# Performance work log

Hardware: AMD Instinct MI355X
Metric: run time of the kernel (lower is better)

## Reference

```python
import jax, jax.numpy as jnp
import numpy as np

N_HEAD = 16
D_HEAD = 64
D_MODEL = 1024
D_INNER = 4096
QLEN = 1024
MLEN = 1024
BSZ = 2
LN_EPS = 1e-5


def _layer_norm(x, g, b, eps=LN_EPS):
    mu = jnp.mean(x, axis=-1, keepdims=True)
    var = jnp.var(x, axis=-1, keepdims=True)
    return (x - mu) * jax.lax.rsqrt(var + eps) * g + b


def _rel_shift(x):
    # x: [qlen, rlen, bsz, n_head]
    q, r, b, n = x.shape
    zp = jnp.zeros((q, 1, b, n), x.dtype)
    xp = jnp.concatenate([zp, x], axis=1).reshape(r + 1, q, b, n)
    return xp[1:].reshape(q, r, b, n)


def setup_inputs() -> dict:
    key = jax.random.key(0)
    ks = jax.random.split(key, 12)
    klen = MLEN + QLEN
    w = jax.random.normal(ks[0], (QLEN, BSZ, D_MODEL), jnp.float32)
    r = jax.random.normal(ks[1], (klen, D_MODEL), jnp.float32)
    mems = jax.random.normal(ks[2], (MLEN, BSZ, D_MODEL), jnp.float32)
    # causal mask: query i attends keys j <= i + mlen
    i = jnp.arange(QLEN)[:, None]
    j = jnp.arange(klen)[None, :]
    attn_mask = (j > i + MLEN)[:, :, None]  # [qlen, klen, 1] bool
    s = 0.02
    params = dict(
        qkv_w=jax.random.normal(ks[3], (3 * N_HEAD * D_HEAD, D_MODEL), jnp.float32) * s,
        r_net_w=jax.random.normal(ks[4], (N_HEAD * D_HEAD, D_MODEL), jnp.float32) * s,
        o_w=jax.random.normal(ks[5], (D_MODEL, N_HEAD * D_HEAD), jnp.float32) * s,
        r_r_bias=jax.random.normal(ks[6], (N_HEAD, D_HEAD), jnp.float32) * s,
        r_w_bias=jax.random.normal(ks[7], (N_HEAD, D_HEAD), jnp.float32) * s,
        ln1_g=jnp.ones((D_MODEL,), jnp.float32),
        ln1_b=jnp.zeros((D_MODEL,), jnp.float32),
        ff_w1=jax.random.normal(ks[8], (D_INNER, D_MODEL), jnp.float32) * s,
        ff_b1=jnp.zeros((D_INNER,), jnp.float32),
        ff_w2=jax.random.normal(ks[9], (D_MODEL, D_INNER), jnp.float32) * s,
        ff_b2=jnp.zeros((D_MODEL,), jnp.float32),
        ln2_g=jnp.ones((D_MODEL,), jnp.float32),
        ln2_b=jnp.zeros((D_MODEL,), jnp.float32),
    )
    return dict(w=w, r=r, mems=mems, attn_mask=attn_mask, **params)


def reference(w, r, mems, attn_mask, qkv_w, r_net_w, o_w, r_r_bias, r_w_bias,
              ln1_g, ln1_b, ff_w1, ff_b1, ff_w2, ff_b2, ln2_g, ln2_b):
    qlen, bsz = w.shape[0], w.shape[1]
    scale = 1.0 / (D_HEAD ** 0.5)
    cat = jnp.concatenate([mems, w], axis=0)              # [klen, b, d_model]
    klen = cat.shape[0]
    w_heads = cat @ qkv_w.T                                # [klen, b, 3*n*d]
    wq, wk, wv = jnp.split(w_heads, 3, axis=-1)
    wq = wq[-qlen:]
    r_head_k = (r @ r_net_w.T).reshape(-1, N_HEAD, D_HEAD)  # [rlen, n, d]
    wq = wq.reshape(qlen, bsz, N_HEAD, D_HEAD)
    wk = wk.reshape(klen, bsz, N_HEAD, D_HEAD)
    wv = wv.reshape(klen, bsz, N_HEAD, D_HEAD)
    AC = jnp.einsum('ibnd,jbnd->ijbn', wq + r_w_bias, wk)   # content term
    BD = jnp.einsum('ibnd,jnd->ijbn', wq + r_r_bias, r_head_k)
    BD = _rel_shift(BD)                                     # position term
    attn_score = (AC + BD) * scale
    mask_value = jnp.finfo(attn_score.dtype).min
    attn_score = jnp.where(attn_mask[:, :, :, None], mask_value, attn_score)
    attn_prob = jax.nn.softmax(attn_score, axis=1)
    attn_vec = jnp.einsum('ijbn,jbnd->ibnd', attn_prob, wv)
    attn_vec = attn_vec.reshape(qlen, bsz, N_HEAD * D_HEAD)
    attn_out = attn_vec @ o_w.T
    h = _layer_norm(w + attn_out, ln1_g, ln1_b)             # post-lnorm
    core = jax.nn.relu(h @ ff_w1.T + ff_b1) @ ff_w2.T + ff_b2
    out = _layer_norm(h + core, ln2_g, ln2_b)
    return out
```

## Files before the change

kernel.cpp:

```cpp
#include <hip/hip_runtime.h>
#include <math.h>

#define QLEN 1024
#define MLEN 1024
#define KLEN 2048
#define BSZc 2
#define NH 16
#define DH 64
#define DM 1024
#define DI 4096

typedef unsigned short ushort_t;
typedef __attribute__((ext_vector_type(8))) short short8;
typedef __attribute__((ext_vector_type(4))) float f32x4;

__device__ __forceinline__ ushort_t f2bf(float x) {
    unsigned int u = __float_as_uint(x);
    unsigned int r = (u + 0x7FFFu + ((u >> 16) & 1u)) >> 16;
    return (ushort_t)r;
}

__device__ __forceinline__ void gload_lds16(const ushort_t* g, ushort_t* l) {
    __builtin_amdgcn_global_load_lds(
        (const __attribute__((address_space(1))) unsigned int*)g,
        (__attribute__((address_space(3))) unsigned int*)l,
        16, 0, 0);
}

__device__ __forceinline__ void cast8(const float* s, ushort_t* d, int g) {
    const float4 a = *(const float4*)(s + g * 8);
    const float4 b = *(const float4*)(s + g * 8 + 4);
    short8 o;
    o[0] = (short)f2bf(a.x); o[1] = (short)f2bf(a.y);
    o[2] = (short)f2bf(a.z); o[3] = (short)f2bf(a.w);
    o[4] = (short)f2bf(b.x); o[5] = (short)f2bf(b.y);
    o[6] = (short)f2bf(b.z); o[7] = (short)f2bf(b.w);
    *(short8*)(d + g * 8) = o;
}

__global__ __launch_bounds__(256)
void cast_phase1(const float* __restrict__ qkv_w, const float* __restrict__ rnet_w,
                 const float* __restrict__ mems, const float* __restrict__ w,
                 const float* __restrict__ r,
                 ushort_t* __restrict__ W1, ushort_t* __restrict__ W2,
                 ushort_t* __restrict__ Acat, ushort_t* __restrict__ Rsrc)
{
    int g = blockIdx.x * 256 + threadIdx.x;
    if (g < 393216)            { cast8(qkv_w,  W1,              g); }
    else if (g < 524288)       { cast8(rnet_w, W2,              g - 393216); }
    else if (g < 786432)       { cast8(mems,   Acat,            g - 524288); }
    else if (g < 1048576)      { cast8(w,      Acat + 2097152,  g - 786432); }
    else if (g < 1310720)      { cast8(r,      Rsrc,            g - 1048576); }
}

__global__ __launch_bounds__(256)
void cast_phase2(const float* __restrict__ o_w, const float* __restrict__ ffw1,
                 const float* __restrict__ ffw2,
                 ushort_t* __restrict__ W3, ushort_t* __restrict__ W4,
                 ushort_t* __restrict__ W5)
{
    int g = blockIdx.x * 256 + threadIdx.x;
    if (g < 131072)            { cast8(o_w,  W3, g); }
    else if (g < 655360)       { cast8(ffw1, W4, g - 131072); }
    else if (g < 1179648)      { cast8(ffw2, W5, g - 655360); }
}

template<int EMODE, int ACT, int BN, int SPLIT>
__global__ __launch_bounds__(256)
void gemm_mfma(const ushort_t* __restrict__ A, const ushort_t* __restrict__ B,
               const float* __restrict__ bias,
               void* __restrict__ O0v, void* __restrict__ O1v,
               int M, int N, int Ks, int lda, int ldb)
{
    constexpr int JT = BN / 32;
    __shared__ ushort_t At0[128 * 32];
    __shared__ ushort_t At1[128 * 32];
    __shared__ ushort_t Bt0[BN * 32];
    __shared__ ushort_t Bt1[BN * 32];

    const int tid  = threadIdx.x;
    const int lane = tid & 63;
    const int w    = tid >> 6;
    const int lr   = lane & 15;
    const int quad = lane >> 4;
    const int m0   = blockIdx.x * 128;
    const int n0   = blockIdx.y * BN;
    const int z    = (SPLIT > 1) ? (int)blockIdx.z : 0;
    const int kbase = z * Ks;
    const int wm0  = (w >> 1) * 64;
    const int wn0  = (w & 1) * (BN / 2);

    f32x4 acc[4][JT];
#pragma unroll
    for (int it = 0; it < 4; ++it)
#pragma unroll
        for (int jt = 0; jt < JT; ++jt) acc[it][jt] = (f32x4){0.f, 0.f, 0.f, 0.f};

    const int srow = lane >> 2;
    const int scol = (lane & 3) << 3;
    const ushort_t* Ag = A + (size_t)(m0 + w * 32 + srow) * lda + kbase + scol;
    ushort_t* a00 = At0 + (w * 32) * 32;
    ushort_t* a01 = At0 + (w * 32 + 16) * 32;
    ushort_t* a10 = At1 + (w * 32) * 32;
    ushort_t* a11 = At1 + (w * 32 + 16) * 32;
    const ushort_t* Bg;
    ushort_t *b00, *b01 = nullptr, *b10, *b11 = nullptr;
    if (BN == 128) {
        Bg  = B + (size_t)(n0 + w * 32 + srow) * ldb + kbase + scol;
        b00 = Bt0 + (w * 32) * 32;
        b01 = Bt0 + (w * 32 + 16) * 32;
        b10 = Bt1 + (w * 32) * 32;
        b11 = Bt1 + (w * 32 + 16) * 32;
    } else {
        Bg  = B + (size_t)(n0 + w * 16 + srow) * ldb + kbase + scol;
        b00 = Bt0 + (w * 16) * 32;
        b10 = Bt1 + (w * 16) * 32;
    }

    const ushort_t* Ato0 = At0 + (wm0 + lr) * 32 + quad * 8;
    const ushort_t* Ato1 = At1 + (wm0 + lr) * 32 + quad * 8;
    const ushort_t* Bto0 = Bt0 + (wn0 + lr) * 32 + quad * 8;
    const ushort_t* Bto1 = Bt1 + (wn0 + lr) * 32 + quad * 8;

    for (int k0 = 0; k0 < Ks; k0 += 64) {
        __syncthreads();
        gload_lds16(Ag + k0, a00);
        gload_lds16(Ag + (size_t)16 * lda + k0, a01);
        gload_lds16(Ag + k0 + 32, a10);
        gload_lds16(Ag + (size_t)16 * lda + k0 + 32, a11);
        if (BN == 128) {
            gload_lds16(Bg + k0, b00);
            gload_lds16(Bg + (size_t)16 * ldb + k0, b01);
            gload_lds16(Bg + k0 + 32, b10);
            gload_lds16(Bg + (size_t)16 * ldb + k0 + 32, b11);
        } else {
            gload_lds16(Bg + k0, b00);
            gload_lds16(Bg + k0 + 32, b10);
        }
        __syncthreads();

        short8 af[4], bf[JT];
#pragma unroll
        for (int it = 0; it < 4; ++it)
            af[it] = *(const short8*)(Ato0 + it * 16 * 32);
#pragma unroll
        for (int jt = 0; jt < JT; ++jt)
            bf[jt] = *(const short8*)(Bto0 + jt * 16 * 32);
#pragma unroll
        for (int it = 0; it < 4; ++it)
#pragma unroll
            for (int jt = 0; jt < JT; ++jt)
                acc[it][jt] = __builtin_amdgcn_mfma_f32_16x16x32_bf16(
                    af[it], bf[jt], acc[it][jt], 0, 0, 0);
#pragma unroll
        for (int it = 0; it < 4; ++it)
            af[it] = *(const short8*)(Ato1 + it * 16 * 32);
#pragma unroll
        for (int jt = 0; jt < JT; ++jt)
            bf[jt] = *(const short8*)(Bto1 + jt * 16 * 32);
#pragma unroll
        for (int it = 0; it < 4; ++it)
#pragma unroll
            for (int jt = 0; jt < JT; ++jt)
                acc[it][jt] = __builtin_amdgcn_mfma_f32_16x16x32_bf16(
                    af[it], bf[jt], acc[it][jt], 0, 0, 0);
    }

#pragma unroll
    for (int it = 0; it < 4; ++it)
#pragma unroll
        for (int jt = 0; jt < JT; ++jt)
#pragma unroll
            for (int rg = 0; rg < 4; ++rg) {
                const int m = m0 + wm0 + it * 16 + quad * 4 + rg;
                const int n = n0 + wn0 + jt * 16 + lr;
                float v = acc[it][jt][rg];
                if (EMODE == 0) {
                    float* dst = (float*)(z ? O1v : O0v);
                    if (bias && z == 0) v += bias[n];
                    dst[(size_t)m * N + n] = v;
                } else {
                    v += bias[n];
                    if (ACT == 1) v = fmaxf(v, 0.f);
                    ((ushort_t*)O0v)[(size_t)m * N + n] = f2bf(v);
                }
            }
}

__global__ __launch_bounds__(256)
void gemm_qkvr(const ushort_t* __restrict__ Acat, const ushort_t* __restrict__ W1,
               const ushort_t* __restrict__ Rsrc, const ushort_t* __restrict__ W2,
               ushort_t* __restrict__ Qac, ushort_t* __restrict__ Qbd,
               ushort_t* __restrict__ Kbf, ushort_t* __restrict__ Vtb,
               ushort_t* __restrict__ Rh,
               const float* __restrict__ rwb, const float* __restrict__ rrb)
{
    __shared__ ushort_t At0[128 * 32];
    __shared__ ushort_t At1[128 * 32];
    __shared__ ushort_t Bt0[128 * 32];
    __shared__ ushort_t Bt1[128 * 32];

    const int bid  = blockIdx.x;
    const bool isr = bid >= 768;
    const ushort_t* A; const ushort_t* B; int m0, n0;
    if (!isr) { A = Acat; B = W1; m0 = (bid & 31) * 128; n0 = (bid >> 5) * 128; }
    else { int t = bid - 768; A = Rsrc; B = W2; m0 = (t & 15) * 128; n0 = (t >> 4) * 128; }
    const int K = 1024;

    const int tid  = threadIdx.x;
    const int lane = tid & 63;
    const int w    = tid >> 6;
    const int lr   = lane & 15;
    const int quad = lane >> 4;
    const int wm0  = (w >> 1) * 64;
    const int wn0  = (w & 1) * 64;

    f32x4 acc[4][4];
#pragma unroll
    for (int it = 0; it < 4; ++it)
#pragma unroll
        for (int jt = 0; jt < 4; ++jt) acc[it][jt] = (f32x4){0.f, 0.f, 0.f, 0.f};

    const int srow = lane >> 2;
    const int scol = (lane & 3) << 3;
    const ushort_t* Ag = A + (size_t)(m0 + w * 32 + srow) * K + scol;
    const ushort_t* Bg = B + (size_t)(n0 + w * 32 + srow) * K + scol;
    ushort_t* a00 = At0 + (w * 32) * 32;
    ushort_t* a01 = At0 + (w * 32 + 16) * 32;
    ushort_t* a10 = At1 + (w * 32) * 32;
    ushort_t* a11 = At1 + (w * 32 + 16) * 32;
    ushort_t* b00 = Bt0 + (w * 32) * 32;
    ushort_t* b01 = Bt0 + (w * 32 + 16) * 32;
    ushort_t* b10 = Bt1 + (w * 32) * 32;
    ushort_t* b11 = Bt1 + (w * 32 + 16) * 32;

    const ushort_t* Ato0 = At0 + (wm0 + lr) * 32 + quad * 8;
    const ushort_t* Ato1 = At1 + (wm0 + lr) * 32 + quad * 8;
    const ushort_t* Bto0 = Bt0 + (wn0 + lr) * 32 + quad * 8;
    const ushort_t* Bto1 = Bt1 + (wn0 + lr) * 32 + quad * 8;

    for (int k0 = 0; k0 < K; k0 += 64) {
        __syncthreads();
        gload_lds16(Ag + k0, a00);
        gload_lds16(Ag + (size_t)16 * K + k0, a01);
        gload_lds16(Ag + k0 + 32, a10);
        gload_lds16(Ag + (size_t)16 * K + k0 + 32, a11);
        gload_lds16(Bg + k0, b00);
        gload_lds16(Bg + (size_t)16 * K + k0, b01);
        gload_lds16(Bg + k0 + 32, b10);
        gload_lds16(Bg + (size_t)16 * K + k0 + 32, b11);
        __syncthreads();

        short8 af[4], bf[4];
#pragma unroll
        for (int it = 0; it < 4; ++it)
            af[it] = *(const short8*)(Ato0 + it * 16 * 32);
#pragma unroll
        for (int jt = 0; jt < 4; ++jt)
            bf[jt] = *(const short8*)(Bto0 + jt * 16 * 32);
#pragma unroll
        for (int it = 0; it < 4; ++it)
#pragma unroll
            for (int jt = 0; jt < 4; ++jt)
                acc[it][jt] = __builtin_amdgcn_mfma_f32_16x16x32_bf16(
                    af[it], bf[jt], acc[it][jt], 0, 0, 0);
#pragma unroll
        for (int it = 0; it < 4; ++it)
            af[it] = *(const short8*)(Ato1 + it * 16 * 32);
#pragma unroll
        for (int jt = 0; jt < 4; ++jt)
            bf[jt] = *(const short8*)(Bto1 + jt * 16 * 32);
#pragma unroll
        for (int it = 0; it < 4; ++it)
#pragma unroll
            for (int jt = 0; jt < 4; ++jt)
                acc[it][jt] = __builtin_amdgcn_mfma_f32_16x16x32_bf16(
                    af[it], bf[jt], acc[it][jt], 0, 0, 0);
    }

#pragma unroll
    for (int it = 0; it < 4; ++it)
#pragma unroll
        for (int jt = 0; jt < 4; ++jt)
#pragma unroll
            for (int rg = 0; rg < 4; ++rg) {
                const int m = m0 + wm0 + it * 16 + quad * 4 + rg;
                const int n = n0 + wn0 + jt * 16 + lr;
                const float v = acc[it][jt][rg];
                if (!isr) {
                    const int j = m >> 1, b = m & 1;
                    const int part = n >> 10, hh = (n >> 6) & 15, d = n & 63;
                    if (part == 0) {
                        if (j >= MLEN) {
                            const int qi = j - MLEN;
                            const size_t qidx = (((size_t)(b * NH + hh)) * QLEN + qi) * DH + d;
                            Qac[qidx] = f2bf(v + rwb[hh * DH + d]);
                            Qbd[qidx] = f2bf(v + rrb[hh * DH + d]);
                        }
                    } else if (part == 1) {
                        Kbf[(((size_t)(b * NH + hh)) * KLEN + j) * DH + d] = f2bf(v);
                    } else {
                        Vtb[(((size_t)(b * NH + hh)) * DH + d) * KLEN + j] = f2bf(v);
                    }
                } else {
                    const int hh = n >> 6, d = n & 63;
                    Rh[(((size_t)hh) * KLEN + m) * DH + d] = f2bf(v);
                }
            }
}

__global__ __launch_bounds__(256, 3)
void attn_mfma(const ushort_t* __restrict__ Qac, const ushort_t* __restrict__ Qbd,
               const ushort_t* __restrict__ Kb, const ushort_t* __restrict__ Vt,
               const ushort_t* __restrict__ Rb,
               float* __restrict__ OpA, float* __restrict__ OpB,
               float* __restrict__ Mp, float* __restrict__ Lp)
{
    __shared__ __align__(16) ushort_t Kt[64 * 64];
    __shared__ __align__(16) ushort_t Rt[128 * 64];
    __shared__ __align__(16) float    Bw[4][16][84];

    const int tid  = threadIdx.x;
    const int lane = tid & 63;
    const int w    = tid >> 6;
    const int lr   = lane & 15;
    const int quad = lane >> 4;
    const int d    = blockIdx.x;
    const int L    = (d & 7) * 224 + (d >> 3);
    const int bh   = L / 56;
    const int r    = L % 56;
    int qt, z;
    if (r < 32) { qt = 15 - (r >> 2); z = r & 3; }
    else        { int r2 = r - 32; int q3 = r2 / 3; qt = 7 - q3; z = r2 - q3 * 3; }
    const int i0   = qt << 6;
    const int h    = bh & 15;
    const int b    = bh >> 4;

    short8 qaf[2], qbf[2];
    {
        const size_t rowoff = ((size_t)bh * QLEN + i0 + w * 16 + lr) * DH;
#pragma unroll
        for (int kt = 0; kt < 2; ++kt) {
            qaf[kt] = *(const short8*)(Qac + rowoff + kt * 32 + quad * 8);
            qbf[kt] = *(const short8*)(Qbd + rowoff + kt * 32 + quad * 8);
        }
    }

    f32x4 O[4];
#pragma unroll
    for (int nt = 0; nt < 4; ++nt) O[nt] = (f32x4){0.f, 0.f, 0.f, 0.f};
    float m_run = -3.4e38f, l_run = 0.f;

    const int nc   = qt + 17;
    const int c_lo = z * 8;
    const int c_hi = (c_lo + 8 < nc) ? (c_lo + 8) : nc;
    const int stw  = 3 - w;
    const float SC = 0.125f * 1.44269504f;
    const ushort_t* Kh  = Kb + (size_t)bh * KLEN * DH;
    const ushort_t* Vh  = Vt + (size_t)bh * DH * KLEN;
    const ushort_t* Rhp = Rb + (size_t)h * KLEN * DH;

    const int lrow = lane >> 3;
    const int lsg  = lane & 7;
    const int sgo  = (lsg ^ lrow) << 3;
    const int xq   = lr & 7;
    const int fo0  = ((quad ^ xq)) << 3;
    const int fo1  = (((4 | quad) ^ xq)) << 3;

    {
        const int j0 = c_lo << 6;
        const int wb = 960 - i0 + j0;
#pragma unroll
        for (int t = 0; t < 2; ++t) {
            const int rb  = t * 32 + w * 8;
            gload_lds16(Kh + (size_t)(j0 + rb + lrow) * DH + sgo,
                        Kt + rb * 64);
        }
#pragma unroll
        for (int t = 0; t < 4; ++t) {
            const int gb = wb + t * 32 + w * 8;
            const int g  = gb + lrow;
            const int gc = g > (KLEN - 1) ? (KLEN - 1) : g;
            gload_lds16(Rhp + (size_t)gc * DH + sgo,
                        Rt + (gb & 127) * 64);
        }
    }

    for (int c = c_lo; c < c_hi; ++c) {
        const int j0 = c << 6;
        const int wb = 960 - i0 + j0;

        __syncthreads();

        short8 vpf[2][4];
#pragma unroll
        for (int kt = 0; kt < 2; ++kt)
#pragma unroll
            for (int nt = 0; nt < 4; ++nt)
                vpf[kt][nt] = *(const short8*)(
                    Vh + (size_t)(nt * 16 + lr) * KLEN + j0 + kt * 32 + quad * 8);

#pragma unroll
        for (int ctl = 0; ctl < 5; ++ctl) {
            const int wr = (stw + ctl) * 16 + lr;
            const int ring = (wb + wr) & 127;
            f32x4 zz = (f32x4){0.f, 0.f, 0.f, 0.f};
            short8 r0 = *(const short8*)&Rt[ring * 64 + fo0];
            zz = __builtin_amdgcn_mfma_f32_16x16x32_bf16(qbf[0], r0, zz, 0, 0, 0);
            short8 r1 = *(const short8*)&Rt[ring * 64 + fo1];
            zz = __builtin_amdgcn_mfma_f32_16x16x32_bf16(qbf[1], r1, zz, 0, 0, 0);
#pragma unroll
            for (int rg = 0; rg < 4; ++rg)
                Bw[w][quad * 4 + rg][ctl * 16 + lr] = zz[rg];
        }
#pragma unroll
        for (int ct = 0; ct < 4; ++ct) {
            f32x4 zz = (f32x4){0.f, 0.f, 0.f, 0.f};
            short8 k0f = *(const short8*)&Kt[(ct * 16 + lr) * 64 + fo0];
            zz = __builtin_amdgcn_mfma_f32_16x16x32_bf16(qaf[0], k0f, zz, 0, 0, 0);
            short8 k1f = *(const short8*)&Kt[(ct * 16 + lr) * 64 + fo1];
            zz = __builtin_amdgcn_mfma_f32_16x16x32_bf16(qaf[1], k1f, zz, 0, 0, 0);
#pragma unroll
            for (int rg = 0; rg < 4; ++rg) {
                const int rrow = quad * 4 + rg;
                Bw[w][rrow][ct * 16 + lr + 15 - rrow] += zz[rg];
            }
        }

        const int lim = i0 + w * 16 + lr + 1024 - j0;
        float pv[16];
        float mx = -3.4e38f;
#pragma unroll
        for (int kt = 0; kt < 2; ++kt)
#pragma unroll
            for (int t = 0; t < 8; ++t) {
                const int jj = kt * 32 + quad * 8 + t;
                float sv = Bw[w][lr][jj + 15 - lr] * SC;
                sv = (jj > lim) ? -3.4e38f : sv;
                pv[kt * 8 + t] = sv;
                mx = fmaxf(mx, sv);
            }
        mx = fmaxf(mx, __shfl_xor(mx, 16, 64));
        mx = fmaxf(mx, __shfl_xor(mx, 32, 64));
        const float m_new = fmaxf(m_run, mx);
        float ps = 0.f;
        short8 pf[2];
#pragma unroll
        for (int kt = 0; kt < 2; ++kt)
#pragma unroll
            for (int t = 0; t < 8; ++t) {
                const float e = exp2f(pv[kt * 8 + t] - m_new);
                ps += e;
                pf[kt][t] = (short)f2bf(e);
            }
        ps += __shfl_xor(ps, 16, 64);
        ps += __shfl_xor(ps, 32, 64);
        const float alpha = exp2f(m_run - m_new);
        m_run = m_new;
        l_run = l_run * alpha + ps;

        __syncthreads();

        if (c + 1 < c_hi) {
            const int j1 = j0 + 64;
#pragma unroll
            for (int t = 0; t < 2; ++t) {
                const int rb = t * 32 + w * 8;
                gload_lds16(Kh + (size_t)(j1 + rb + lrow) * DH + sgo,
                            Kt + rb * 64);
            }
#pragma unroll
            for (int t = 0; t < 2; ++t) {
                const int gb = wb + 128 + t * 32 + w * 8;
                const int g  = gb + lrow;
                const int gc = g > (KLEN - 1) ? (KLEN - 1) : g;
                gload_lds16(Rhp + (size_t)gc * DH + sgo,
                            Rt + (gb & 127) * 64);
            }
        }

        float ar[4];
#pragma unroll
        for (int rg = 0; rg < 4; ++rg)
            ar[rg] = __shfl(alpha, quad * 4 + rg, 64);
#pragma unroll
        for (int nt = 0; nt < 4; ++nt) {
            O[nt][0] *= ar[0]; O[nt][1] *= ar[1];
            O[nt][2] *= ar[2]; O[nt][3] *= ar[3];
        }
#pragma unroll
        for (int kt = 0; kt < 2; ++kt)
#pragma unroll
            for (int nt = 0; nt < 4; ++nt)
                O[nt] = __builtin_amdgcn_mfma_f32_16x16x32_bf16(pf[kt], vpf[kt][nt], O[nt], 0, 0, 0);
    }

    if (quad == 0) {
        const size_t mi = ((size_t)(z * 32 + bh)) * QLEN + i0 + w * 16 + lr;
        Mp[mi] = m_run;
        Lp[mi] = l_run;
    }
    float* Op = (z < 2) ? (OpA + (size_t)z * 2097152)
                        : (OpB + (size_t)(z - 2) * 2097152);
#pragma unroll
    for (int nt = 0; nt < 4; ++nt)
#pragma unroll
        for (int rg = 0; rg < 4; ++rg) {
            const int i = i0 + w * 16 + quad * 4 + rg;
            Op[((size_t)i * BSZc + b) * DM + h * DH + nt * 16 + lr] = O[nt][rg];
        }
}

__global__ __launch_bounds__(256)
void attn_merge(const float* __restrict__ OpA, const float* __restrict__ OpB,
                const float* __restrict__ Mp, const float* __restrict__ Lp,
                ushort_t* __restrict__ AV)
{
    const int row = blockIdx.x;
    const int tid = threadIdx.x;
    const int i = row >> 1, b = row & 1;
    const int h = tid >> 4;
    const int bh = b * NH + h;
    const size_t mi = (size_t)bh * QLEN + i;
    const bool p4 = (i >= 512);
    const float m0 = Mp[mi],                l0 = Lp[mi];
    const float m1 = Mp[32 * QLEN + mi],    l1 = Lp[32 * QLEN + mi];
    const float m2 = Mp[64 * QLEN + mi],    l2 = Lp[64 * QLEN + mi];
    float m3 = -3.4e38f, l3 = 0.f;
    if (p4) { m3 = Mp[96 * QLEN + mi]; l3 = Lp[96 * QLEN + mi]; }
    const float M = fmaxf(fmaxf(m0, m1), fmaxf(m2, m3));
    const float a0 = exp2f(m0 - M), a1 = exp2f(m1 - M);
    const float a2 = exp2f(m2 - M), a3 = exp2f(m3 - M);
    const float rl = 1.f / (l0 * a0 + l1 * a1 + l2 * a2 + l3 * a3);
    const float f0 = a0 * rl, f1 = a1 * rl, f2 = a2 * rl, f3 = a3 * rl;
    const float4 o0 = ((const float4*)(OpA + (size_t)row * DM))[tid];
    const float4 o1 = ((const float4*)(OpA + 2097152 + (size_t)row * DM))[tid];
    const float4 o2 = ((const float4*)(OpB + (size_t)row * DM))[tid];
    float4 o3 = (float4){0.f, 0.f, 0.f, 0.f};
    if (p4) o3 = ((const float4*)(OpB + 2097152 + (size_t)row * DM))[tid];
    ushort_t* p = AV + (size_t)row * DM + tid * 4;
    p[0] = f2bf(o0.x * f0 + o1.x * f1 + o2.x * f2 + o3.x * f3);
    p[1] = f2bf(o0.y * f0 + o1.y * f1 + o2.y * f2 + o3.y * f3);
    p[2] = f2bf(o0.z * f0 + o1.z * f1 + o2.z * f2 + o3.z * f3);
    p[3] = f2bf(o0.w * f0 + o1.w * f1 + o2.w * f2 + o3.w * f3);
}

__global__ __launch_bounds__(256)
void add_ln(const float* __restrict__ X, const float* __restrict__ Y0,
            const float* __restrict__ Y1,
            const float* __restrict__ gg, const float* __restrict__ bb,
            float* __restrict__ out, ushort_t* __restrict__ outb)
{
    const int row  = blockIdx.x;
    const int tid  = threadIdx.x;
    const int lane = tid & 63;
    const int w    = tid >> 6;
    __shared__ float ssum[4], ssq[4];

    const float4 xv = ((const float4*)(X + (size_t)row * DM))[tid];
    const float4 yv = ((const float4*)(Y0 + (size_t)row * DM))[tid];
    float v0 = xv.x + yv.x, v1 = xv.y + yv.y;
    float v2 = xv.z + yv.z, v3 = xv.w + yv.w;
    if (Y1) {
        const float4 zv = ((const float4*)(Y1 + (size_t)row * DM))[tid];
        v0 += zv.x; v1 += zv.y; v2 += zv.z; v3 += zv.w;
    }
    float s = v0 + v1 + v2 + v3;
    float q = v0 * v0 + v1 * v1 + v2 * v2 + v3 * v3;
#pragma unroll
    for (int off = 32; off > 0; off >>= 1) {
        s += __shfl_xor(s, off, 64);
        q += __shfl_xor(q, off, 64);
    }
    if (lane == 0) { ssum[w] = s; ssq[w] = q; }
    __syncthreads();
    s = ssum[0] + ssum[1] + ssum[2] + ssum[3];
    q = ssq[0] + ssq[1] + ssq[2] + ssq[3];
    const float mean = s * (1.f / DM);
    const float var  = q * (1.f / DM) - mean * mean;
    const float rs   = rsqrtf(var + 1e-5f);
    const float4 g4 = ((const float4*)gg)[tid];
    const float4 b4 = ((const float4*)bb)[tid];
    float4 ov;
    ov.x = (v0 - mean) * rs * g4.x + b4.x;
    ov.y = (v1 - mean) * rs * g4.y + b4.y;
    ov.z = (v2 - mean) * rs * g4.z + b4.z;
    ov.w = (v3 - mean) * rs * g4.w + b4.w;
    ((float4*)(out + (size_t)row * DM))[tid] = ov;
    if (outb) {
        ushort_t* p = outb + (size_t)row * DM + tid * 4;
        p[0] = f2bf(ov.x); p[1] = f2bf(ov.y);
        p[2] = f2bf(ov.z); p[3] = f2bf(ov.w);
    }
}

extern "C" void kernel_launch(void* const* d_in, const int* in_sizes, int n_in,
                              void* d_out, int out_size, void* d_ws, size_t ws_size,
                              hipStream_t stream)
{
    (void)in_sizes; (void)n_in; (void)out_size; (void)ws_size;
    const float* w      = (const float*)d_in[0];
    const float* r      = (const float*)d_in[1];
    const float* mems   = (const float*)d_in[2];
    const float* qkv_w  = (const float*)d_in[4];
    const float* rnet_w = (const float*)d_in[5];
    const float* o_w    = (const float*)d_in[6];
    const float* r_r_b  = (const float*)d_in[7];
    const float* r_w_b  = (const float*)d_in[8];
    const float* ln1g   = (const float*)d_in[9];
    const float* ln1b   = (const float*)d_in[10];
    const float* ffw1   = (const float*)d_in[11];
    const float* ffb1   = (const float*)d_in[12];
    const float* ffw2   = (const float*)d_in[13];
    const float* ffb2   = (const float*)d_in[14];
    const float* ln2g   = (const float*)d_in[15];
    const float* ln2b   = (const float*)d_in[16];
    float* out = (float*)d_out;

    char* wsb = (char*)d_ws;
    const size_t MB = 1024 * 1024;
    ushort_t* W1    = (ushort_t*)(wsb + 0 * MB);
    ushort_t* W2    = (ushort_t*)(wsb + 6 * MB);
    ushort_t* Acat  = (ushort_t*)(wsb + 8 * MB);
    ushort_t* Rsrc  = (ushort_t*)(wsb + 16 * MB);
    ushort_t* Qac   = (ushort_t*)(wsb + 20 * MB);
    ushort_t* Qbd   = (ushort_t*)(wsb + 24 * MB);
    ushort_t* Kbf   = (ushort_t*)(wsb + 28 * MB);
    ushort_t* Vt    = (ushort_t*)(wsb + 36 * MB);
    ushort_t* Rh    = (ushort_t*)(wsb + 44 * MB);
    float*    OpA   = (float*)(wsb + 0 * MB);
    float*    OpB   = (float*)(wsb + 48 * MB);
    float*    Mp    = (float*)(wsb + 16 * MB);
    float*    Lp    = (float*)(wsb + 16 * MB + 512 * 1024);
    ushort_t* AVec  = (ushort_t*)(wsb + 18 * MB);
    ushort_t* W3    = (ushort_t*)(wsb + 4 * MB);
    float*    AOut0 = (float*)(wsb + 8 * MB);
    float*    AOut1 = (float*)(wsb + 44 * MB);
    float*    Hbuf  = (float*)(wsb + 16 * MB);
    ushort_t* Hbf   = (ushort_t*)(wsb + 24 * MB);
    ushort_t* W4    = (ushort_t*)(wsb + 28 * MB);
    ushort_t* FFbf  = (ushort_t*)(wsb + 36 * MB);
    ushort_t* W5    = (ushort_t*)(wsb + 52 * MB);
    float*    Core0 = (float*)(wsb + 0 * MB);
    float*    Core1 = (float*)(wsb + 8 * MB);

    dim3 blk(256);

    cast_phase1<<<dim3(5120), blk, 0, stream>>>(qkv_w, rnet_w, mems, w, r,
                                                W1, W2, Acat, Rsrc);

    gemm_qkvr<<<dim3(896), blk, 0, stream>>>(
        Acat, W1, Rsrc, W2, Qac, Qbd, Kbf, Vt, Rh, r_w_b, r_r_b);

    attn_mfma<<<dim3(1792), blk, 0, stream>>>(
        Qac, Qbd, Kbf, Vt, Rh, OpA, OpB, Mp, Lp);

    attn_merge<<<dim3(2048), blk, 0, stream>>>(OpA, OpB, Mp, Lp, AVec);

    cast_phase2<<<dim3(4608), blk, 0, stream>>>(o_w, ffw1, ffw2, W3, W4, W5);

    gemm_mfma<0, 0, 64, 2><<<dim3(16, 16, 2), blk, 0, stream>>>(
        AVec, W3, nullptr, AOut0, AOut1, 2048, 1024, 512, 1024, 1024);

    add_ln<<<dim3(2 * QLEN), blk, 0, stream>>>(w, AOut0, AOut1, ln1g, ln1b, Hbuf, Hbf);

    gemm_mfma<3, 1, 128, 1><<<dim3(16, 32), blk, 0, stream>>>(
        Hbf, W4, ffb1, FFbf, nullptr, 2048, 4096, 1024, 1024, 1024);

    gemm_mfma<0, 0, 64, 2><<<dim3(16, 16, 2), blk, 0, stream>>>(
        FFbf, W5, ffb2, Core0, Core1, 2048, 1024, 2048, 4096, 4096);

    add_ln<<<dim3(2 * QLEN), blk, 0, stream>>>(Hbuf, Core0, Core1, ln2g, ln2b, out, nullptr);
}
```

Before: 380.6 us.

## Double-buffer LDS tiles to prefetch next K-slice during MFMA compute

Both GEMM kernels previously loaded a 64-wide K chunk into two LDS halves and then computed, with two barriers per iteration and no overlap between loads and math. They now use a ping-pong buffer of 32-wide K slices: the next slice is issued with global_load_lds while MFMAs run on the current one, with a single barrier per step. This aims to hide global memory latency. The cost is twice as many loop iterations with less work per barrier, and correctness depends on the barrier making the async LDS loads visible before use.

```diff
diff --git a/kernel.cpp b/kernel.cpp
--- a/kernel.cpp
+++ b/kernel.cpp
@@ -73,10 +73,8 @@
                int M, int N, int Ks, int lda, int ldb)
 {
     constexpr int JT = BN / 32;
-    __shared__ ushort_t At0[128 * 32];
-    __shared__ ushort_t At1[128 * 32];
-    __shared__ ushort_t Bt0[BN * 32];
-    __shared__ ushort_t Bt1[BN * 32];
+    __shared__ ushort_t At[2][128 * 32];
+    __shared__ ushort_t Bt[2][BN * 32];
 
     const int tid  = threadIdx.x;
     const int lane = tid & 63;
@@ -99,71 +97,47 @@
     const int srow = lane >> 2;
     const int scol = (lane & 3) << 3;
     const ushort_t* Ag = A + (size_t)(m0 + w * 32 + srow) * lda + kbase + scol;
-    ushort_t* a00 = At0 + (w * 32) * 32;
-    ushort_t* a01 = At0 + (w * 32 + 16) * 32;
-    ushort_t* a10 = At1 + (w * 32) * 32;
-    ushort_t* a11 = At1 + (w * 32 + 16) * 32;
-    const ushort_t* Bg;
-    ushort_t *b00, *b01 = nullptr, *b10, *b11 = nullptr;
-    if (BN == 128) {
-        Bg  = B + (size_t)(n0 + w * 32 + srow) * ldb + kbase + scol;
-        b00 = Bt0 + (w * 32) * 32;
-        b01 = Bt0 + (w * 32 + 16) * 32;
-        b10 = Bt1 + (w * 32) * 32;
-        b11 = Bt1 + (w * 32 + 16) * 32;
-    } else {
-        Bg  = B + (size_t)(n0 + w * 16 + srow) * ldb + kbase + scol;
-        b00 = Bt0 + (w * 16) * 32;
-        b10 = Bt1 + (w * 16) * 32;
-    }
-
-    const ushort_t* Ato0 = At0 + (wm0 + lr) * 32 + quad * 8;
-    const ushort_t* Ato1 = At1 + (wm0 + lr) * 32 + quad * 8;
-    const ushort_t* Bto0 = Bt0 + (wn0 + lr) * 32 + quad * 8;
-    const ushort_t* Bto1 = Bt1 + (wn0 + lr) * 32 + quad * 8;
-
-    for (int k0 = 0; k0 < Ks; k0 += 64) {
-        __syncthreads();
-        gload_lds16(Ag + k0, a00);
-        gload_lds16(Ag + (size_t)16 * lda + k0, a01);
-        gload_lds16(Ag + k0 + 32, a10);
-        gload_lds16(Ag + (size_t)16 * lda + k0 + 32, a11);
+    const ushort_t* Bg = (BN == 128)
+        ? B + (size_t)(n0 + w * 32 + srow) * ldb + kbase + scol
+        : B + (size_t)(n0 + w * 16 + srow) * ldb + kbase + scol;
+
+    auto stage = [&](int kk, int buf) {
+        gload_lds16(Ag + kk,                    &At[buf][(w * 32) * 32]);
+        gload_lds16(Ag + (size_t)16 * lda + kk, &At[buf][(w * 32 + 16) * 32]);
         if (BN == 128) {
-            gload_lds16(Bg + k0, b00);
-            gload_lds16(Bg + (size_t)16 * ldb + k0, b01);
-            gload_lds16(Bg + k0 + 32, b10);
-            gload_lds16(Bg + (size_t)16 * ldb + k0 + 32, b11);
+            gload_lds16(Bg + kk,                    &Bt[buf][(w * 32) * 32]);
+            gload_lds16(Bg + (size_t)16 * ldb + kk, &Bt[buf][(w * 32 + 16) * 32]);
         } else {
-            gload_lds16(Bg + k0, b00);
-            gload_lds16(Bg + k0 + 32, b10);
-        }
-        __syncthreads();
-
+            gload_lds16(Bg + kk,                    &Bt[buf][(w * 16) * 32]);
+        }
+    };
+
+    stage(0, 0);
+    __syncthreads();
+
+    const int nsteps = Ks >> 5;
+    int cur = 0;
+    for (int s = 0; s < nsteps; ++s) {
+        if (s + 1 < nsteps) stage((s + 1) << 5, cur ^ 1);
+
+        const ushort_t* Ato = &At[cur][(wm0 + lr) * 32 + quad * 8];
+        const ushort_t* Bto = &Bt[cur][(wn0 + lr) * 32 + quad * 8];
         short8 af[4], bf[JT];
 #pragma unroll
         for (int it = 0; it < 4; ++it)
-            af[it] = *(const short8*)(Ato0 + it * 16 * 32);
+            af[it] = *(const short8*)(Ato + it * 16 * 32);
 #pragma unroll
         for (int jt = 0; jt < JT; ++jt)
-            bf[jt] = *(const short8*)(Bto0 + jt * 16 * 32);
+            bf[jt] = *(const short8*)(Bto + jt * 16 * 32);
 #pragma unroll
         for (int it = 0; it < 4; ++it)
 #pragma unroll
             for (int jt = 0; jt < JT; ++jt)
                 acc[it][jt] = __builtin_amdgcn_mfma_f32_16x16x32_bf16(
                     af[it], bf[jt], acc[it][jt], 0, 0, 0);
-#pragma unroll
-        for (int it = 0; it < 4; ++it)
-            af[it] = *(const short8*)(Ato1 + it * 16 * 32);
-#pragma unroll
-        for (int jt = 0; jt < JT; ++jt)
-            bf[jt] = *(const short8*)(Bto1 + jt * 16 * 32);
-#pragma unroll
-        for (int it = 0; it < 4; ++it)
-#pragma unroll
-            for (int jt = 0; jt < JT; ++jt)
-                acc[it][jt] = __builtin_amdgcn_mfma_f32_16x16x32_bf16(
-                    af[it], bf[jt], acc[it][jt], 0, 0, 0);
+
+        __syncthreads();
+        cur ^= 1;
     }
 
 #pragma unroll
@@ -195,10 +169,8 @@
                ushort_t* __restrict__ Rh,
                const float* __restrict__ rwb, const float* __restrict__ rrb)
 {
-    __shared__ ushort_t At0[128 * 32];
-    __shared__ ushort_t At1[128 * 32];
-    __shared__ ushort_t Bt0[128 * 32];
-    __shared__ ushort_t Bt1[128 * 32];
+    __shared__ ushort_t At[2][128 * 32];
+    __shared__ ushort_t Bt[2][128 * 32];
 
     const int bid  = blockIdx.x;
     const bool isr = bid >= 768;
@@ -225,57 +197,39 @@
     const int scol = (lane & 3) << 3;
     const ushort_t* Ag = A + (size_t)(m0 + w * 32 + srow) * K + scol;
     const ushort_t* Bg = B + (size_t)(n0 + w * 32 + srow) * K + scol;
-    ushort_t* a00 = At0 + (w * 32) * 32;
-    ushort_t* a01 = At0 + (w * 32 + 16) * 32;
-    ushort_t* a10 = At1 + (w * 32) * 32;
-    ushort_t* a11 = At1 + (w * 32 + 16) * 32;
-    ushort_t* b00 = Bt0 + (w * 32) * 32;
-    ushort_t* b01 = Bt0 + (w * 32 + 16) * 32;
-    ushort_t* b10 = Bt1 + (w * 32) * 32;
-    ushort_t* b11 = Bt1 + (w * 32 + 16) * 32;
-
-    const ushort_t* Ato0 = At0 + (wm0 + lr) * 32 + quad * 8;
-    const ushort_t* Ato1 = At1 + (wm0 + lr) * 32 + quad * 8;
-    const ushort_t* Bto0 = Bt0 + (wn0 + lr) * 32 + quad * 8;
-    const ushort_t* Bto1 = Bt1 + (wn0 + lr) * 32 + quad * 8;
-
-    for (int k0 = 0; k0 < K; k0 += 64) {
-        __syncthreads();
-        gload_lds16(Ag + k0, a00);
-        gload_lds16(Ag + (size_t)16 * K + k0, a01);
-        gload_lds16(Ag + k0 + 32, a10);
-        gload_lds16(Ag + (size_t)16 * K + k0 + 32, a11);
-        gload_lds16(Bg + k0, b00);
-        gload_lds16(Bg + (size_t)16 * K + k0, b01);
-        gload_lds16(Bg + k0 + 32, b10);
-        gload_lds16(Bg + (size_t)16 * K + k0 + 32, b11);
-        __syncthreads();
-
+
+    auto stage = [&](int kk, int buf) {
+        gload_lds16(Ag + kk,                  &At[buf][(w * 32) * 32]);
+        gload_lds16(Ag + (size_t)16 * K + kk, &At[buf][(w * 32 + 16) * 32]);
+        gload_lds16(Bg + kk,                  &Bt[buf][(w * 32) * 32]);
+        gload_lds16(Bg + (size_t)16 * K + kk, &Bt[buf][(w * 32 + 16) * 32]);
+    };
+
+    stage(0, 0);
+    __syncthreads();
+
+    int cur = 0;
+    for (int s = 0; s < 32; ++s) {
+        if (s + 1 < 32) stage((s + 1) << 5, cur ^ 1);
+
+        const ushort_t* Ato = &At[cur][(wm0 + lr) * 32 + quad * 8];
+        const ushort_t* Bto = &Bt[cur][(wn0 + lr) * 32 + quad * 8];
         short8 af[4], bf[4];
 #pragma unroll
         for (int it = 0; it < 4; ++it)
-            af[it] = *(const short8*)(Ato0 + it * 16 * 32);
+            af[it] = *(const short8*)(Ato + it * 16 * 32);
 #pragma unroll
         for (int jt = 0; jt < 4; ++jt)
-            bf[jt] = *(const short8*)(Bto0 + jt * 16 * 32);
+            bf[jt] = *(const short8*)(Bto + jt * 16 * 32);
 #pragma unroll
         for (int it = 0; it < 4; ++it)
 #pragma unroll
             for (int jt = 0; jt < 4; ++jt)
                 acc[it][jt] = __builtin_amdgcn_mfma_f32_16x16x32_bf16(
                     af[it], bf[jt], acc[it][jt], 0, 0, 0);
-#pragma unroll
-        for (int it = 0; it < 4; ++it)
-            af[it] = *(const short8*)(Ato1 + it * 16 * 32);
-#pragma unroll
-        for (int jt = 0; jt < 4; ++jt)
-            bf[jt] = *(const short8*)(Bto1 + jt * 16 * 32);
-#pragma unroll
-        for (int it = 0; it < 4; ++it)
-#pragma unroll
-            for (int jt = 0; jt < 4; ++jt)
-                acc[it][jt] = __builtin_amdgcn_mfma_f32_16x16x32_bf16(
-                    af[it], bf[jt], acc[it][jt], 0, 0, 0);
+
+        __syncthreads();
+        cur ^= 1;
     }
 
 #pragma unroll
```

After: 389.4 us. 1.02x slower.
